# Optimization experiments

Hardware: AMD Instinct MI355X
Metric: run time of the kernel (lower is better)

## Reference

```python
import jax, jax.numpy as jnp
import numpy as np

N_HEAD = 16

def apply_rope(t, cos, sin):
    # t: [B, H, T, hd]; cos/sin: [T, hd//2] -> broadcast [1,1,T,hd//2]
    hd = t.shape[-1]
    t1, t2 = t[..., : hd // 2], t[..., hd // 2 :]
    c = cos[None, None, :, :]
    s = sin[None, None, :, :]
    return jnp.concatenate([t1 * c - t2 * s, t1 * s + t2 * c], axis=-1)

def setup_inputs() -> dict:
    key = jax.random.key(0)
    k1, k2, k3, k4, k5 = jax.random.split(key, 5)
    B, T, C = 2, 2048, 2048
    hd = C // N_HEAD
    x = jax.random.normal(k1, (B, T, C), dtype=jnp.float32)
    cos = jax.random.uniform(k2, (T, hd // 2), dtype=jnp.float32)
    sin = jax.random.uniform(k3, (T, hd // 2), dtype=jnp.float32)
    W_attn = jax.random.normal(k4, (C, 3 * C), dtype=jnp.float32) * (1.0 / np.sqrt(C))
    W_proj = jax.random.normal(k5, (C, C), dtype=jnp.float32) * (1.0 / np.sqrt(C))
    return {"x": x, "cos": cos, "sin": sin, "W_attn": W_attn, "W_proj": W_proj}

def reference(x, cos, sin, W_attn, W_proj):
    B, T, C = x.shape
    hd = C // N_HEAD
    qkv = jnp.einsum("btc,cd->btd", x, W_attn)  # [B,T,3C]
    q, k, v = jnp.split(qkv, 3, axis=-1)
    # [B,T,C] -> [B,H,T,hd]
    def to_heads(t):
        return t.reshape(B, T, N_HEAD, hd).transpose(0, 2, 1, 3)
    q, k, v = to_heads(q), to_heads(k), to_heads(v)
    q = apply_rope(q, cos[:T], sin[:T])
    k = apply_rope(k, cos[:T], sin[:T])
    scale = 1.0 / np.sqrt(hd).astype(np.float32)
    scores = jnp.einsum("bhqd,bhkd->bhqk", q, k) * scale
    causal = jnp.tril(jnp.ones((T, T), dtype=bool))
    scores = jnp.where(causal[None, None], scores, jnp.finfo(scores.dtype).min)
    attn = jax.nn.softmax(scores, axis=-1)
    y = jnp.einsum("bhqk,bhkd->bhqd", attn, v)  # [B,H,T,hd]
    y = y.transpose(0, 2, 1, 3).reshape(B, T, C)
    return jnp.einsum("btc,cd->btd", y, W_proj)
```

## Files before the change

kernel.cpp:

```cpp
#include <hip/hip_runtime.h>
#include <stdint.h>

typedef unsigned short u16;
typedef __bf16 v8bf __attribute__((ext_vector_type(8)));
typedef float f32x4 __attribute__((ext_vector_type(4)));

#define MFMA16(a, b, c) __builtin_amdgcn_mfma_f32_16x16x32_bf16((a), (b), (c), 0, 0, 0)

typedef const __attribute__((address_space(1))) uint32_t* gp32;
typedef __attribute__((address_space(3))) uint32_t* lp32;
#define ASYNC16(g, l) __builtin_amdgcn_global_load_lds((gp32)(const void*)(g), (lp32)(void*)(l), 16, 0, 0)

__device__ __forceinline__ u16 f2bf(float f) {
  union { float f; uint32_t u; } v; v.f = f;
  uint32_t r = v.u + 0x7fffu + ((v.u >> 16) & 1u);
  return (u16)(r >> 16);
}
__device__ __forceinline__ float bf2f(u16 h) {
  union { uint32_t u; float f; } v; v.u = ((uint32_t)h) << 16;
  return v.f;
}

__device__ __forceinline__ int swK(int r, int lc) {
  return r * 128 + (((lc ^ (r & 7)) & 15) << 3);
}
__device__ __forceinline__ int swV(int r, int lc) {
  return r * 64 + (((lc ^ (r & 7)) & 7) << 3);
}

__global__ __launch_bounds__(256) void cast_x_kernel(const float* __restrict__ in,
                                                     u16* __restrict__ out) {
  int i = (blockIdx.x * 256 + threadIdx.x) * 8;
  float4 a = *(const float4*)(in + i);
  float4 b = *(const float4*)(in + i + 4);
  uint4 o;
  o.x = (uint32_t)f2bf(a.x) | ((uint32_t)f2bf(a.y) << 16);
  o.y = (uint32_t)f2bf(a.z) | ((uint32_t)f2bf(a.w) << 16);
  o.z = (uint32_t)f2bf(b.x) | ((uint32_t)f2bf(b.y) << 16);
  o.w = (uint32_t)f2bf(b.z) | ((uint32_t)f2bf(b.w) << 16);
  *(uint4*)(out + i) = o;
}

__global__ __launch_bounds__(256) void transpose_cast_kernel(const float* __restrict__ in,
                                                             u16* __restrict__ out,
                                                             int R, int Cc) {
  __shared__ u16 tile[32][34];
  int c0 = blockIdx.x * 32, r0 = blockIdx.y * 32;
  int tx = threadIdx.x, ty = threadIdx.y;
#pragma unroll
  for (int i = 0; i < 32; i += 8)
    tile[ty + i][tx] = f2bf(in[(size_t)(r0 + ty + i) * Cc + c0 + tx]);
  __syncthreads();
#pragma unroll
  for (int i = 0; i < 32; i += 8)
    out[(size_t)(c0 + ty + i) * R + r0 + tx] = tile[tx][ty + i];
}

template <typename OutT>
__global__ __launch_bounds__(256) void gemm_bt(const u16* __restrict__ A,
                                               const u16* __restrict__ Bt,
                                               OutT* __restrict__ C, int M, int N, int K) {
  __shared__ u16 As[128 * 64];
  __shared__ u16 Bs[128 * 64];
  int tid = threadIdx.x;
  int wave = tid >> 6, lane = tid & 63, quad = lane >> 4, l16 = lane & 15;
  int wr = wave >> 1, wc = wave & 1;
  int m0 = blockIdx.y * 128, n0 = blockIdx.x * 128;
  f32x4 acc[4][4] = {};
  int lrow = lane >> 3, lk = lane & 7;
  int lc = lk ^ lrow;
  const u16* Ab = A + (size_t)m0 * K;
  const u16* Bb = Bt + (size_t)n0 * K;

  for (int k0 = 0; k0 < K; k0 += 64) {
#pragma unroll
    for (int j = 0; j < 4; ++j) {
      int rbase = wave * 32 + j * 8;
      int row = rbase + lrow;
      ASYNC16(Ab + (size_t)row * K + k0 + lc * 8, &As[rbase * 64]);
      ASYNC16(Bb + (size_t)row * K + k0 + lc * 8, &Bs[rbase * 64]);
    }
    __syncthreads();
#pragma unroll
    for (int ks = 0; ks < 2; ++ks) {
      v8bf af[4], bfr[4];
#pragma unroll
      for (int t = 0; t < 4; ++t) {
        af[t]  = *(const v8bf*)&As[swV(wr * 64 + t * 16 + l16, ks * 4 + quad)];
        bfr[t] = *(const v8bf*)&Bs[swV(wc * 64 + t * 16 + l16, ks * 4 + quad)];
      }
#pragma unroll
      for (int mt = 0; mt < 4; ++mt)
#pragma unroll
        for (int nt = 0; nt < 4; ++nt)
          acc[mt][nt] = MFMA16(af[mt], bfr[nt], acc[mt][nt]);
    }
    __syncthreads();
  }
#pragma unroll
  for (int mt = 0; mt < 4; ++mt)
#pragma unroll
    for (int nt = 0; nt < 4; ++nt) {
      int row = m0 + wr * 64 + mt * 16 + quad * 4;
      int col = n0 + wc * 64 + nt * 16 + l16;
#pragma unroll
      for (int r = 0; r < 4; ++r) {
        float v = acc[mt][nt][r];
        if constexpr (sizeof(OutT) == 2)
          C[(size_t)(row + r) * N + col] = (OutT)f2bf(v);
        else
          C[(size_t)(row + r) * N + col] = v;
      }
    }
}

__global__ __launch_bounds__(256) void rope_repack(const u16* __restrict__ qkv,
                                                   const float* __restrict__ cosp,
                                                   const float* __restrict__ sinp,
                                                   u16* __restrict__ qh, u16* __restrict__ kh,
                                                   u16* __restrict__ vt) {
  __shared__ u16 tile[128 * 130];
  const int T = 2048, C3 = 6144;
  const float QSCL = 0.08838834764831845f * 1.4426950408889634f;
  int t0 = blockIdx.x * 128;
  int bh = blockIdx.y, b = bh >> 4, h = bh & 15;
  int tid = threadIdx.x;
#pragma unroll 2
  for (int i = 0; i < 32; ++i) {
    int e = i * 256 + tid;
    int tl = e >> 6, j = e & 63;
    int t = t0 + tl;
    size_t base = (size_t)(b * T + t) * C3 + h * 128;
    float c = cosp[t * 64 + j], s = sinp[t * 64 + j];
    float q1 = bf2f(qkv[base + j]),        q2 = bf2f(qkv[base + 64 + j]);
    float k1 = bf2f(qkv[base + 2048 + j]), k2 = bf2f(qkv[base + 2048 + 64 + j]);
    size_t o = ((size_t)bh * T + t) * 128;
    qh[o + j]      = f2bf((q1 * c - q2 * s) * QSCL);
    qh[o + 64 + j] = f2bf((q1 * s + q2 * c) * QSCL);
    kh[o + j]      = f2bf(k1 * c - k2 * s);
    kh[o + 64 + j] = f2bf(k1 * s + k2 * c);
  }
#pragma unroll 2
  for (int i = 0; i < 32; ++i) {
    int e = i * 256 + tid;
    int tl = e >> 6, dc = (e & 63) * 2;
    size_t base = (size_t)(b * T + t0 + tl) * C3 + 4096 + h * 128;
    *(uint32_t*)&tile[tl * 130 + dc] = *(const uint32_t*)&qkv[base + dc];
  }
  __syncthreads();
#pragma unroll 2
  for (int i = 0; i < 32; ++i) {
    int e = i * 256 + tid;
    int d = e >> 6, tp = (e & 63) * 2;
    uint32_t v = (uint32_t)tile[tp * 130 + d] | ((uint32_t)tile[(tp + 1) * 130 + d] << 16);
    *(uint32_t*)&vt[((size_t)bh * 128 + d) * T + t0 + tp] = v;
  }
}

__global__ __launch_bounds__(256) void flash_attn(const u16* __restrict__ qh,
                                                  const u16* __restrict__ kh,
                                                  const u16* __restrict__ vt,
                                                  u16* __restrict__ yh) {
  __shared__ u16 Ks[2][64 * 128];
  __shared__ u16 Vs[128 * 64];
  __shared__ u16 Pb[128 * 64];
  const int T = 2048, HD = 128;
  int tid = threadIdx.x;
  int wave = tid >> 6, lane = tid & 63, quad = lane >> 4, l16 = lane & 15;
  int bh = blockIdx.y, b = bh >> 4, h = bh & 15;
  const u16* qb = qh + (size_t)bh * T * HD;
  const u16* kb = kh + (size_t)bh * T * HD;
  const u16* vb = vt + (size_t)bh * HD * T;
  int krow_off = lane >> 4, kchunk = lane & 15;
  int vrow_off = lane >> 3, vchunk = lane & 7;

  for (int tp = 0; tp < 2; ++tp) {
    int qt = tp ? 15 - (int)blockIdx.x : (int)blockIdx.x;
    int q0 = qt * 128;
    int n_it = 2 * qt + 2;

    v8bf qf[2][4];
#pragma unroll
    for (int mt = 0; mt < 2; ++mt)
#pragma unroll
      for (int ks = 0; ks < 4; ++ks)
        qf[mt][ks] = *(const v8bf*)&qb[(size_t)(q0 + wave * 32 + mt * 16 + l16) * HD + ks * 32 + quad * 8];

    f32x4 acc[2][8] = {};
    float rs_p[2][4] = {};
    uint4 vreg[4];

#pragma unroll
    for (int j = 0; j < 4; ++j) {
      int rbase = wave * 16 + j * 4;
      int r = rbase + krow_off;
      int lc = kchunk ^ (r & 7);
      ASYNC16(kb + (size_t)r * HD + lc * 8, &Ks[0][rbase * 128]);
    }
#pragma unroll
    for (int j = 0; j < 4; ++j) {
      int row = wave * 32 + j * 8 + vrow_off;
      int lc = vchunk ^ (row & 7);
      vreg[j] = *(const uint4*)&vb[(size_t)row * T + lc * 8];
    }
    __syncthreads();
#pragma unroll
    for (int j = 0; j < 4; ++j) {
      int row = wave * 32 + j * 8 + vrow_off;
      *(uint4*)&Vs[row * 64 + vchunk * 8] = vreg[j];
    }

    for (int it = 0; it < n_it; ++it) {
      int c = it & 1;
      __syncthreads();

      if (it + 1 < n_it) {
        int kv0n = (it + 1) * 64;
#pragma unroll
        for (int j = 0; j < 4; ++j) {
          int rbase = wave * 16 + j * 4;
          int r = rbase + krow_off;
          int lc = kchunk ^ (r & 7);
          ASYNC16(kb + (size_t)(kv0n + r) * HD + lc * 8, &Ks[1 - c][rbase * 128]);
        }
#pragma unroll
        for (int j = 0; j < 4; ++j) {
          int row = wave * 32 + j * 8 + vrow_off;
          int lc = vchunk ^ (row & 7);
          vreg[j] = *(const uint4*)&vb[(size_t)row * T + kv0n + lc * 8];
        }
      }

      f32x4 s[2][4] = {};
#pragma unroll
      for (int ks = 0; ks < 4; ++ks)
#pragma unroll
        for (int nt = 0; nt < 4; ++nt) {
          v8bf kf = *(const v8bf*)&Ks[c][swK(nt * 16 + l16, ks * 4 + quad)];
          s[0][nt] = MFMA16(qf[0][ks], kf, s[0][nt]);
          s[1][nt] = MFMA16(qf[1][ks], kf, s[1][nt]);
        }

      if (it >= 2 * qt) {
        int kv0 = it * 64;
#pragma unroll
        for (int mt = 0; mt < 2; ++mt)
#pragma unroll
          for (int r = 0; r < 4; ++r) {
            int row = q0 + wave * 32 + mt * 16 + quad * 4 + r;
#pragma unroll
            for (int nt = 0; nt < 4; ++nt)
              if (kv0 + nt * 16 + l16 > row) s[mt][nt][r] = -1e30f;
          }
      }

#pragma unroll
      for (int mt = 0; mt < 2; ++mt)
#pragma unroll
        for (int nt = 0; nt < 4; ++nt)
#pragma unroll
          for (int r = 0; r < 4; ++r) {
            float p = __builtin_exp2f(s[mt][nt][r]);
            rs_p[mt][r] += p;
            int row = wave * 32 + mt * 16 + quad * 4 + r;
            int col = nt * 16 + l16;
            Pb[row * 64 + ((((col >> 3) ^ (row & 7)) & 7) << 3) + (col & 7)] = f2bf(p);
          }

#pragma unroll
      for (int ks = 0; ks < 2; ++ks) {
        v8bf pa0 = *(const v8bf*)&Pb[swV(wave * 32 + l16, ks * 4 + quad)];
        v8bf pa1 = *(const v8bf*)&Pb[swV(wave * 32 + 16 + l16, ks * 4 + quad)];
#pragma unroll
        for (int dt = 0; dt < 8; ++dt) {
          v8bf vf = *(const v8bf*)&Vs[swV(dt * 16 + l16, ks * 4 + quad)];
          acc[0][dt] = MFMA16(pa0, vf, acc[0][dt]);
          acc[1][dt] = MFMA16(pa1, vf, acc[1][dt]);
        }
      }

      __syncthreads();

      if (it + 1 < n_it) {
#pragma unroll
        for (int j = 0; j < 4; ++j) {
          int row = wave * 32 + j * 8 + vrow_off;
          *(uint4*)&Vs[row * 64 + vchunk * 8] = vreg[j];
        }
      }
    }

#pragma unroll
    for (int mt = 0; mt < 2; ++mt)
#pragma unroll
      for (int r = 0; r < 4; ++r) {
        float rsv = rs_p[mt][r];
        rsv += __shfl_xor(rsv, 1);
        rsv += __shfl_xor(rsv, 2);
        rsv += __shfl_xor(rsv, 4);
        rsv += __shfl_xor(rsv, 8);
        float inv = 1.f / rsv;
        int t = q0 + wave * 32 + mt * 16 + quad * 4 + r;
#pragma unroll
        for (int dt = 0; dt < 8; ++dt)
          yh[(size_t)(b * T + t) * 2048 + h * 128 + dt * 16 + l16] = f2bf(acc[mt][dt][r] * inv);
      }
  }
}

extern "C" void kernel_launch(void* const* d_in, const int* in_sizes, int n_in,
                              void* d_out, int out_size, void* d_ws, size_t ws_size,
                              hipStream_t stream) {
  const float* x    = (const float*)d_in[0];
  const float* cosp = (const float*)d_in[1];
  const float* sinp = (const float*)d_in[2];
  const float* Wa   = (const float*)d_in[3];
  const float* Wp   = (const float*)d_in[4];
  float* out = (float*)d_out;

  char* ws = (char*)d_ws;
  u16* xb  = (u16*)(ws);
  u16* WaT = (u16*)(ws + (size_t)(16 << 20));
  u16* WpT = (u16*)(ws + (size_t)(40 << 20));
  u16* qkv = (u16*)(ws + (size_t)(48 << 20));
  u16* qh  = (u16*)(ws + (size_t)(96 << 20));
  u16* kh  = (u16*)(ws + (size_t)(112 << 20));
  u16* vt  = (u16*)(ws + (size_t)(128 << 20));
  u16* yh  = (u16*)(ws + (size_t)(144 << 20));

  cast_x_kernel<<<4096, 256, 0, stream>>>(x, xb);
  transpose_cast_kernel<<<dim3(192, 64), dim3(32, 8), 0, stream>>>(Wa, WaT, 2048, 6144);
  transpose_cast_kernel<<<dim3(64, 64), dim3(32, 8), 0, stream>>>(Wp, WpT, 2048, 2048);
  gemm_bt<u16><<<dim3(48, 32), 256, 0, stream>>>(xb, WaT, qkv, 4096, 6144, 2048);
  rope_repack<<<dim3(16, 32), 256, 0, stream>>>(qkv, cosp, sinp, qh, kh, vt);
  flash_attn<<<dim3(8, 32), 256, 0, stream>>>(qh, kh, vt, yh);
  gemm_bt<float><<<dim3(16, 32), 256, 0, stream>>>(yh, WpT, out, 4096, 2048, 2048);
}
```

Baseline: 448.6 us.

## Use 8 waves per flash-attention block with 16 query rows per wave

The flash attention kernel now launches 512 threads (8 waves) per block instead of 256. Each wave owns 16 query rows instead of 32, and the cooperative K/V tile loads are split across twice as many waves. The aim is to cut per-wave register pressure and raise latency hiding on the same 128-row query tile. The cost is that each K fragment read from LDS now feeds only one MFMA instead of two, so LDS traffic per flop doubles, and barriers must synchronize more waves.

```diff
diff --git a/kernel.cpp b/kernel.cpp
--- a/kernel.cpp
+++ b/kernel.cpp
@@ -157,7 +157,7 @@
   }
 }
 
-__global__ __launch_bounds__(256) void flash_attn(const u16* __restrict__ qh,
+__global__ __launch_bounds__(512) void flash_attn(const u16* __restrict__ qh,
                                                   const u16* __restrict__ kh,
                                                   const u16* __restrict__ vt,
                                                   u16* __restrict__ yh) {
@@ -179,34 +179,32 @@
     int q0 = qt * 128;
     int n_it = 2 * qt + 2;
 
-    v8bf qf[2][4];
-#pragma unroll
-    for (int mt = 0; mt < 2; ++mt)
-#pragma unroll
-      for (int ks = 0; ks < 4; ++ks)
-        qf[mt][ks] = *(const v8bf*)&qb[(size_t)(q0 + wave * 32 + mt * 16 + l16) * HD + ks * 32 + quad * 8];
-
-    f32x4 acc[2][8] = {};
-    float rs_p[2][4] = {};
-    uint4 vreg[4];
-
-#pragma unroll
-    for (int j = 0; j < 4; ++j) {
-      int rbase = wave * 16 + j * 4;
+    v8bf qf[4];
+#pragma unroll
+    for (int ks = 0; ks < 4; ++ks)
+      qf[ks] = *(const v8bf*)&qb[(size_t)(q0 + wave * 16 + l16) * HD + ks * 32 + quad * 8];
+
+    f32x4 acc[8] = {};
+    float rs_p[4] = {};
+    uint4 vreg[2];
+
+#pragma unroll
+    for (int j = 0; j < 2; ++j) {
+      int rbase = wave * 8 + j * 4;
       int r = rbase + krow_off;
       int lc = kchunk ^ (r & 7);
       ASYNC16(kb + (size_t)r * HD + lc * 8, &Ks[0][rbase * 128]);
     }
 #pragma unroll
-    for (int j = 0; j < 4; ++j) {
-      int row = wave * 32 + j * 8 + vrow_off;
+    for (int j = 0; j < 2; ++j) {
+      int row = wave * 16 + j * 8 + vrow_off;
       int lc = vchunk ^ (row & 7);
       vreg[j] = *(const uint4*)&vb[(size_t)row * T + lc * 8];
     }
     __syncthreads();
 #pragma unroll
-    for (int j = 0; j < 4; ++j) {
-      int row = wave * 32 + j * 8 + vrow_off;
+    for (int j = 0; j < 2; ++j) {
+      int row = wave * 16 + j * 8 + vrow_off;
       *(uint4*)&Vs[row * 64 + vchunk * 8] = vreg[j];
     }
 
@@ -217,65 +215,58 @@
       if (it + 1 < n_it) {
         int kv0n = (it + 1) * 64;
 #pragma unroll
-        for (int j = 0; j < 4; ++j) {
-          int rbase = wave * 16 + j * 4;
+        for (int j = 0; j < 2; ++j) {
+          int rbase = wave * 8 + j * 4;
           int r = rbase + krow_off;
           int lc = kchunk ^ (r & 7);
           ASYNC16(kb + (size_t)(kv0n + r) * HD + lc * 8, &Ks[1 - c][rbase * 128]);
         }
 #pragma unroll
-        for (int j = 0; j < 4; ++j) {
-          int row = wave * 32 + j * 8 + vrow_off;
+        for (int j = 0; j < 2; ++j) {
+          int row = wave * 16 + j * 8 + vrow_off;
           int lc = vchunk ^ (row & 7);
           vreg[j] = *(const uint4*)&vb[(size_t)row * T + kv0n + lc * 8];
         }
       }
 
-      f32x4 s[2][4] = {};
+      f32x4 s[4] = {};
 #pragma unroll
       for (int ks = 0; ks < 4; ++ks)
 #pragma unroll
         for (int nt = 0; nt < 4; ++nt) {
           v8bf kf = *(const v8bf*)&Ks[c][swK(nt * 16 + l16, ks * 4 + quad)];
-          s[0][nt] = MFMA16(qf[0][ks], kf, s[0][nt]);
-          s[1][nt] = MFMA16(qf[1][ks], kf, s[1][nt]);
+          s[nt] = MFMA16(qf[ks], kf, s[nt]);
         }
 
       if (it >= 2 * qt) {
         int kv0 = it * 64;
 #pragma unroll
-        for (int mt = 0; mt < 2; ++mt)
-#pragma unroll
-          for (int r = 0; r < 4; ++r) {
-            int row = q0 + wave * 32 + mt * 16 + quad * 4 + r;
-#pragma unroll
-            for (int nt = 0; nt < 4; ++nt)
-              if (kv0 + nt * 16 + l16 > row) s[mt][nt][r] = -1e30f;
-          }
-      }
-
-#pragma unroll
-      for (int mt = 0; mt < 2; ++mt)
-#pragma unroll
-        for (int nt = 0; nt < 4; ++nt)
-#pragma unroll
-          for (int r = 0; r < 4; ++r) {
-            float p = __builtin_exp2f(s[mt][nt][r]);
-            rs_p[mt][r] += p;
-            int row = wave * 32 + mt * 16 + quad * 4 + r;
-            int col = nt * 16 + l16;
-            Pb[row * 64 + ((((col >> 3) ^ (row & 7)) & 7) << 3) + (col & 7)] = f2bf(p);
-          }
+        for (int r = 0; r < 4; ++r) {
+          int row = q0 + wave * 16 + quad * 4 + r;
+#pragma unroll
+          for (int nt = 0; nt < 4; ++nt)
+            if (kv0 + nt * 16 + l16 > row) s[nt][r] = -1e30f;
+        }
+      }
+
+#pragma unroll
+      for (int nt = 0; nt < 4; ++nt)
+#pragma unroll
+        for (int r = 0; r < 4; ++r) {
+          float p = __builtin_exp2f(s[nt][r]);
+          rs_p[r] += p;
+          int row = wave * 16 + quad * 4 + r;
+          int col = nt * 16 + l16;
+          Pb[row * 64 + ((((col >> 3) ^ (row & 7)) & 7) << 3) + (col & 7)] = f2bf(p);
+        }
 
 #pragma unroll
       for (int ks = 0; ks < 2; ++ks) {
-        v8bf pa0 = *(const v8bf*)&Pb[swV(wave * 32 + l16, ks * 4 + quad)];
-        v8bf pa1 = *(const v8bf*)&Pb[swV(wave * 32 + 16 + l16, ks * 4 + quad)];
+        v8bf pa = *(const v8bf*)&Pb[swV(wave * 16 + l16, ks * 4 + quad)];
 #pragma unroll
         for (int dt = 0; dt < 8; ++dt) {
           v8bf vf = *(const v8bf*)&Vs[swV(dt * 16 + l16, ks * 4 + quad)];
-          acc[0][dt] = MFMA16(pa0, vf, acc[0][dt]);
-          acc[1][dt] = MFMA16(pa1, vf, acc[1][dt]);
+          acc[dt] = MFMA16(pa, vf, acc[dt]);
         }
       }
 
@@ -283,28 +274,26 @@
 
       if (it + 1 < n_it) {
 #pragma unroll
-        for (int j = 0; j < 4; ++j) {
-          int row = wave * 32 + j * 8 + vrow_off;
+        for (int j = 0; j < 2; ++j) {
+          int row = wave * 16 + j * 8 + vrow_off;
           *(uint4*)&Vs[row * 64 + vchunk * 8] = vreg[j];
         }
       }
     }
 
 #pragma unroll
-    for (int mt = 0; mt < 2; ++mt)
-#pragma unroll
-      for (int r = 0; r < 4; ++r) {
-        float rsv = rs_p[mt][r];
-        rsv += __shfl_xor(rsv, 1);
-        rsv += __shfl_xor(rsv, 2);
-        rsv += __shfl_xor(rsv, 4);
-        rsv += __shfl_xor(rsv, 8);
-        float inv = 1.f / rsv;
-        int t = q0 + wave * 32 + mt * 16 + quad * 4 + r;
-#pragma unroll
-        for (int dt = 0; dt < 8; ++dt)
-          yh[(size_t)(b * T + t) * 2048 + h * 128 + dt * 16 + l16] = f2bf(acc[mt][dt][r] * inv);
-      }
+    for (int r = 0; r < 4; ++r) {
+      float rsv = rs_p[r];
+      rsv += __shfl_xor(rsv, 1);
+      rsv += __shfl_xor(rsv, 2);
+      rsv += __shfl_xor(rsv, 4);
+      rsv += __shfl_xor(rsv, 8);
+      float inv = 1.f / rsv;
+      int t = q0 + wave * 16 + quad * 4 + r;
+#pragma unroll
+      for (int dt = 0; dt < 8; ++dt)
+        yh[(size_t)(b * T + t) * 2048 + h * 128 + dt * 16 + l16] = f2bf(acc[dt][r] * inv);
+    }
   }
 }
 
@@ -333,6 +322,6 @@
   transpose_cast_kernel<<<dim3(64, 64), dim3(32, 8), 0, stream>>>(Wp, WpT, 2048, 2048);
   gemm_bt<u16><<<dim3(48, 32), 256, 0, stream>>>(xb, WaT, qkv, 4096, 6144, 2048);
   rope_repack<<<dim3(16, 32), 256, 0, stream>>>(qkv, cosp, sinp, qh, kh, vt);
-  flash_attn<<<dim3(8, 32), 256, 0, stream>>>(qh, kh, vt, yh);
+  flash_attn<<<dim3(8, 32), 512, 0, stream>>>(qh, kh, vt, yh);
   gemm_bt<float><<<dim3(16, 32), 256, 0, stream>>>(yh, WpT, out, 4096, 2048, 2048);
 }
```

Measured after the change: 423.4 us. 1.06x faster.
